# Kernel tuning notes

Measured on AMD Instinct MI355X. Metric: run time of the kernel, lower is better.

The kernel has to match this reference:

```python
import jax, jax.numpy as jnp
import numpy as np

FRACTION_BITS = 16
INTEGER_BITS = 16
DELTA = 2.0 ** (-(FRACTION_BITS / 2))  # 2^-8
BOUND = 2.0 ** (INTEGER_BITS - 1)      # 2^15


def round_to_fixed(x):
    # floor(x/delta + 0.5), clipped to [-2^15, 2^15-1], rescaled
    rounded = jnp.floor(x / DELTA + 0.5)
    return jnp.clip(rounded, -BOUND, BOUND - 1) * DELTA


def setup_inputs() -> dict:
    key = jax.random.key(0)
    k_x, k_sh, k_sg, k_b = jax.random.split(key, 4)
    N, IN, OUT = 8192, 4096, 4096
    x = jax.random.normal(k_x, (N, IN), dtype=jnp.float32)
    shift = jax.random.uniform(k_sh, (OUT, IN), minval=-10.0, maxval=-1.0, dtype=jnp.float32)
    sign = jax.random.uniform(k_sg, (OUT, IN), minval=-1.0, maxval=0.0, dtype=jnp.float32)
    bound = 1.0 / np.sqrt(IN)
    bias = jax.random.uniform(k_b, (OUT,), minval=-bound, maxval=bound, dtype=jnp.float32)
    return {"x": x, "shift": shift, "sign": sign, "bias": bias}


def reference(x, shift, sign, bias):
    # fixed-point quantization of activations and bias (fallback float path)
    x_q = round_to_fixed(x)
    b_q = round_to_fixed(bias)
    # power-of-two weight: v = 2^round(shift) * (-1)^round(sign)
    v = jnp.exp2(jnp.round(shift)) * jnp.where(jnp.round(sign) % 2 == 0, 1.0, -1.0)
    out = x_q @ v.T + b_q[None, :]
    return out
```

## Files before the change

### kernel.cpp

```cpp
#include <hip/hip_runtime.h>


typedef _Float16 half8 __attribute__((ext_vector_type(8)));
typedef _Float16 half4v __attribute__((ext_vector_type(4)));
typedef float floatx4 __attribute__((ext_vector_type(4)));

__device__ __forceinline__ float qfix(float x) {
    float r = floorf(x * 256.0f + 0.5f);
    r = fminf(fmaxf(r, -32768.0f), 32767.0f);
    return r * 0.00390625f;
}

__global__ __launch_bounds__(256) void quantize_x_kernel(
        const float* __restrict__ x, _Float16* __restrict__ xq, int n4) {
    int i = blockIdx.x * 256 + threadIdx.x;
    const int stride = gridDim.x * 256;
    for (; i < n4; i += stride) {
        float4 v = reinterpret_cast<const float4*>(x)[i];
        half4v o;
        o[0] = (_Float16)qfix(v.x);
        o[1] = (_Float16)qfix(v.y);
        o[2] = (_Float16)qfix(v.z);
        o[3] = (_Float16)qfix(v.w);
        reinterpret_cast<half4v*>(xq)[i] = o;
    }
}

__global__ __launch_bounds__(256) void make_v_kernel(
        const float* __restrict__ shift, const float* __restrict__ sign,
        _Float16* __restrict__ v, int n4) {
    int i = blockIdx.x * 256 + threadIdx.x;
    const int stride = gridDim.x * 256;
    for (; i < n4; i += stride) {
        float4 sh = reinterpret_cast<const float4*>(shift)[i];
        float4 sg = reinterpret_cast<const float4*>(sign)[i];
        half4v o;
        o[0] = (_Float16)ldexpf((rintf(sg.x) == 0.0f) ? 1.0f : -1.0f, (int)rintf(sh.x));
        o[1] = (_Float16)ldexpf((rintf(sg.y) == 0.0f) ? 1.0f : -1.0f, (int)rintf(sh.y));
        o[2] = (_Float16)ldexpf((rintf(sg.z) == 0.0f) ? 1.0f : -1.0f, (int)rintf(sh.z));
        o[3] = (_Float16)ldexpf((rintf(sg.w) == 0.0f) ? 1.0f : -1.0f, (int)rintf(sh.w));
        reinterpret_cast<half4v*>(v)[i] = o;
    }
}

__device__ __forceinline__ void async_load16(const void* g, void* l) {
    __builtin_amdgcn_global_load_lds(
        (const __attribute__((address_space(1))) unsigned int*)g,
        (__attribute__((address_space(3))) unsigned int*)l,
        16, 0, 0);
}

__device__ __forceinline__ void stage_half(const _Float16* __restrict__ G, int ldg,
                                           int row0, int k0, _Float16* lds_half, int t) {
    #pragma unroll
    for (int l = 0; l < 2; ++l) {
        const int r  = l * 64 + (t >> 3);
        const int cb = (t & 7) ^ (r & 7);
        async_load16(G + (size_t)(row0 + r) * ldg + (k0 + cb * 8),
                     lds_half + l * 4096 + t * 8);
    }
}

__device__ __forceinline__ half8 read_frag(const _Float16* hb, int r, int ks, int fko) {
    const int blk = (ks * 4 + fko) ^ (r & 7);
    return *reinterpret_cast<const half8*>(hb + r * 64 + blk * 8);
}

#define MFMA_QUAD(ACCQ, BF)                                               \
    _Pragma("unroll")                                                     \
    for (int mf = 0; mf < 4; ++mf)                                        \
      _Pragma("unroll")                                                   \
      for (int nf = 0; nf < 2; ++nf)                                      \
        _Pragma("unroll")                                                 \
        for (int ks = 0; ks < 2; ++ks)                                    \
          ACCQ[mf][nf] = __builtin_amdgcn_mfma_f32_16x16x32_f16(          \
              af[mf][ks], BF[nf][ks], ACCQ[mf][nf], 0, 0, 0);

#define PHASE_CORE(ACCQ, BF)                                              \
    asm volatile("" ::: "memory");                                        \
    __builtin_amdgcn_s_barrier();                                         \
    __builtin_amdgcn_s_setprio(1);                                        \
    MFMA_QUAD(ACCQ, BF);                                                  \
    __builtin_amdgcn_s_setprio(0);

#define END_BARRIER()                                                     \
    asm volatile("" ::: "memory");                                        \
    __builtin_amdgcn_s_barrier();

#define READ_AF(HALF)                                                     \
    _Pragma("unroll")                                                     \
    for (int mf = 0; mf < 4; ++mf)                                        \
      _Pragma("unroll")                                                   \
      for (int ks = 0; ks < 2; ++ks)                                      \
        af[mf][ks] = read_frag((HALF), wrow * 64 + mf * 16 + fr, ks, fko);

#define READ_BF(DST, HALF)                                                \
    _Pragma("unroll")                                                     \
    for (int nf = 0; nf < 2; ++nf)                                        \
      _Pragma("unroll")                                                   \
      for (int ks = 0; ks < 2; ++ks)                                      \
        DST[nf][ks] = read_frag((HALF), wcol * 32 + nf * 16 + fr, ks, fko);

__global__ __launch_bounds__(512, 2) void gemm8_kernel(
        const _Float16* __restrict__ A,
        const _Float16* __restrict__ B,
        const float* __restrict__ bias,
        float* __restrict__ C,
        int M, int N, int K) {
    extern __shared__ _Float16 smem[];
    const int t = threadIdx.x;
    const int lane = t & 63;
    const int w = t >> 6;
    const int wrow = w >> 2;
    const int wcol = w & 3;
    const int fr  = lane & 15;
    const int fko = lane >> 4;

    const int nwg = gridDim.x;
    const int bid = blockIdx.x;
    const int cpx = nwg >> 3;
    const int swz = (bid & 7) * cpx + (bid >> 3);
    const int ntN = N >> 8;
    const int bm = (swz / ntN) << 8;
    const int bn = (swz % ntN) << 8;

    stage_half(A, K, bm,       0, smem,         t);
    stage_half(B, K, bn,       0, smem + 16384, t);
    stage_half(B, K, bn + 128, 0, smem + 24576, t);
    stage_half(A, K, bm + 128, 0, smem + 8192,  t);
    asm volatile("s_waitcnt vmcnt(0)" ::: "memory");
    __builtin_amdgcn_s_barrier();

    floatx4 acc[2][2][4][2] = {};
    const int NT = K >> 6;

    for (int kt = 0; kt < NT; ++kt) {
        const int cur = kt & 1;
        _Float16* cb = smem + cur * 32768;
        _Float16* nb = smem + (cur ^ 1) * 32768;
        const _Float16* cA0 = cb;
        const _Float16* cA1 = cb + 8192;
        const _Float16* cB0 = cb + 16384;
        const _Float16* cB1 = cb + 24576;
        const int k1 = (kt + 1) << 6;
        const bool more = (kt + 1 < NT);

        half8 af[4][2], bf0[2][2], bf1[2][2];

        READ_AF(cA0);
        READ_BF(bf0, cB0);
        if (more) stage_half(A, K, bm, k1, nb, t);
        PHASE_CORE(acc[0][0], bf0);
        if (more) { asm volatile("s_waitcnt vmcnt(4)" ::: "memory"); }
        else      { asm volatile("s_waitcnt vmcnt(0)" ::: "memory"); }
        END_BARRIER();

        READ_BF(bf1, cB1);
        if (more) stage_half(B, K, bn, k1, nb + 16384, t);
        PHASE_CORE(acc[0][1], bf1);
        if (more) { asm volatile("s_waitcnt vmcnt(4)" ::: "memory"); }
        END_BARRIER();

        READ_AF(cA1);
        if (more) stage_half(B, K, bn + 128, k1, nb + 24576, t);
        PHASE_CORE(acc[1][1], bf1);
        END_BARRIER();

        if (more) stage_half(A, K, bm + 128, k1, nb + 8192, t);
        PHASE_CORE(acc[1][0], bf0);
        if (more) { asm volatile("s_waitcnt vmcnt(4)" ::: "memory"); }
        END_BARRIER();
    }

    #pragma unroll
    for (int qm = 0; qm < 2; ++qm)
      #pragma unroll
      for (int qn = 0; qn < 2; ++qn)
        #pragma unroll
        for (int nf = 0; nf < 2; ++nf) {
            const int gcol = bn + qn * 128 + wcol * 32 + nf * 16 + (lane & 15);
            const float bq = qfix(bias[gcol]);
            #pragma unroll
            for (int mf = 0; mf < 4; ++mf) {
                const int grow = bm + qm * 128 + wrow * 64 + mf * 16 + ((lane >> 4) << 2);
                float* p = C + (size_t)grow * N + gcol;
                #pragma unroll
                for (int r = 0; r < 4; ++r)
                    p[(size_t)r * N] = acc[qm][qn][mf][nf][r] + bq;
            }
        }
}

extern "C" void kernel_launch(void* const* d_in, const int* in_sizes, int n_in,
                              void* d_out, int out_size, void* d_ws, size_t ws_size,
                              hipStream_t stream) {
    const float* x     = (const float*)d_in[0];
    const float* shift = (const float*)d_in[1];
    const float* sign  = (const float*)d_in[2];
    const float* bias  = (const float*)d_in[3];
    float* out = (float*)d_out;

    const int N = in_sizes[3];
    const int K = in_sizes[1] / N;
    const int M = in_sizes[0] / K;

    _Float16* xq = (_Float16*)d_ws;
    _Float16* v  = (_Float16*)((char*)d_ws + (size_t)M * K * sizeof(_Float16));

    quantize_x_kernel<<<2048, 256, 0, stream>>>(x, xq, M * K / 4);
    make_v_kernel<<<2048, 256, 0, stream>>>(shift, sign, v, N * K / 4);

    (void)hipFuncSetAttribute(reinterpret_cast<const void*>(gemm8_kernel),
                              hipFuncAttributeMaxDynamicSharedMemorySize, 131072);
    const int nblk = (M / 256) * (N / 256);
    gemm8_kernel<<<nblk, 512, 131072, stream>>>(xq, v, bias, out, M, N, K);
}
```

Before: 309.8 us.

## Cut per-tile barriers and unroll the K loop by two over static LDS slots

The GEMM main loop now issues fewer workgroup barriers per K tile. The vmcnt waits move in front of the barriers, and the barriers that separated each MFMA phase are dropped. The loop is unrolled by two with fixed ping-pong LDS buffer pointers, so buffer selection arithmetic goes away. The aim is to cut synchronisation stalls between MFMA phases. The cost is a tighter reasoning margin on LDS write-after-read hazards, and the code now assumes an even number of K tiles.

```diff
diff --git a/kernel.cpp b/kernel.cpp
--- a/kernel.cpp
+++ b/kernel.cpp
@@ -76,17 +76,6 @@
           ACCQ[mf][nf] = __builtin_amdgcn_mfma_f32_16x16x32_f16(          \
               af[mf][ks], BF[nf][ks], ACCQ[mf][nf], 0, 0, 0);
 
-#define PHASE_CORE(ACCQ, BF)                                              \
-    asm volatile("" ::: "memory");                                        \
-    __builtin_amdgcn_s_barrier();                                         \
-    __builtin_amdgcn_s_setprio(1);                                        \
-    MFMA_QUAD(ACCQ, BF);                                                  \
-    __builtin_amdgcn_s_setprio(0);
-
-#define END_BARRIER()                                                     \
-    asm volatile("" ::: "memory");                                        \
-    __builtin_amdgcn_s_barrier();
-
 #define READ_AF(HALF)                                                     \
     _Pragma("unroll")                                                     \
     for (int mf = 0; mf < 4; ++mf)                                        \
@@ -100,6 +89,14 @@
       _Pragma("unroll")                                                   \
       for (int ks = 0; ks < 2; ++ks)                                      \
         DST[nf][ks] = read_frag((HALF), wcol * 32 + nf * 16 + fr, ks, fko);
+
+#define VM4()  asm volatile("s_waitcnt vmcnt(4)" ::: "memory")
+#define VM0()  asm volatile("s_waitcnt vmcnt(0)" ::: "memory")
+#define BAR()  __builtin_amdgcn_s_barrier()
+#define PRIO_MFMA(ACCQ, BF)                                               \
+    __builtin_amdgcn_s_setprio(1);                                        \
+    MFMA_QUAD(ACCQ, BF);                                                  \
+    __builtin_amdgcn_s_setprio(0);
 
 __global__ __launch_bounds__(512, 2) void gemm8_kernel(
         const _Float16* __restrict__ A,
@@ -128,48 +125,44 @@
     stage_half(B, K, bn,       0, smem + 16384, t);
     stage_half(B, K, bn + 128, 0, smem + 24576, t);
     stage_half(A, K, bm + 128, 0, smem + 8192,  t);
-    asm volatile("s_waitcnt vmcnt(0)" ::: "memory");
-    __builtin_amdgcn_s_barrier();
+    VM0();
+    BAR();
 
     floatx4 acc[2][2][4][2] = {};
     const int NT = K >> 6;
 
-    for (int kt = 0; kt < NT; ++kt) {
-        const int cur = kt & 1;
-        _Float16* cb = smem + cur * 32768;
-        _Float16* nb = smem + (cur ^ 1) * 32768;
+    auto tile_body = [&](const _Float16* cb, _Float16* nb, int k1, bool more)
+            __attribute__((always_inline)) {
         const _Float16* cA0 = cb;
         const _Float16* cA1 = cb + 8192;
         const _Float16* cB0 = cb + 16384;
         const _Float16* cB1 = cb + 24576;
-        const int k1 = (kt + 1) << 6;
-        const bool more = (kt + 1 < NT);
-
         half8 af[4][2], bf0[2][2], bf1[2][2];
 
         READ_AF(cA0);
         READ_BF(bf0, cB0);
-        if (more) stage_half(A, K, bm, k1, nb, t);
-        PHASE_CORE(acc[0][0], bf0);
-        if (more) { asm volatile("s_waitcnt vmcnt(4)" ::: "memory"); }
-        else      { asm volatile("s_waitcnt vmcnt(0)" ::: "memory"); }
-        END_BARRIER();
+        if (more) { stage_half(A, K, bm, k1, nb, t); VM4(); }
+        else      { VM0(); }
+        BAR();
+        PRIO_MFMA(acc[0][0], bf0);
 
         READ_BF(bf1, cB1);
-        if (more) stage_half(B, K, bn, k1, nb + 16384, t);
-        PHASE_CORE(acc[0][1], bf1);
-        if (more) { asm volatile("s_waitcnt vmcnt(4)" ::: "memory"); }
-        END_BARRIER();
+        if (more) { stage_half(B, K, bn, k1, nb + 16384, t); VM4(); BAR(); }
+        PRIO_MFMA(acc[0][1], bf1);
 
         READ_AF(cA1);
         if (more) stage_half(B, K, bn + 128, k1, nb + 24576, t);
-        PHASE_CORE(acc[1][1], bf1);
-        END_BARRIER();
-
-        if (more) stage_half(A, K, bm + 128, k1, nb + 8192, t);
-        PHASE_CORE(acc[1][0], bf0);
-        if (more) { asm volatile("s_waitcnt vmcnt(4)" ::: "memory"); }
-        END_BARRIER();
+        PRIO_MFMA(acc[1][1], bf1);
+
+        if (more) { stage_half(A, K, bm + 128, k1, nb + 8192, t); VM4(); BAR(); }
+        PRIO_MFMA(acc[1][0], bf0);
+    };
+
+    _Float16* slot0 = smem;
+    _Float16* slot1 = smem + 32768;
+    for (int kt = 0; kt < NT; kt += 2) {
+        tile_body(slot0, slot1, (kt + 1) << 6, true);
+        tile_body(slot1, slot0, (kt + 2) << 6, (kt + 2) < NT);
     }
 
     #pragma unroll
```

After: 363.7 us. +17.4%, slower.
